# Kernel optimization log

Measured on AMD Instinct MI355X. Metric: run time of the kernel, lower is better.

The kernel has to match this reference:

```python
import jax, jax.numpy as jnp
import numpy as np


def setup_inputs() -> dict:
    key = jax.random.key(0)
    k1, k2 = jax.random.split(key)
    B, C, H, W = 8, 19, 512, 1024
    inputs = jax.random.normal(k1, (B, C, H, W), dtype=jnp.float32)
    targets = jax.random.randint(k2, (B, H, W), 0, C, dtype=jnp.int32)
    return {"inputs": inputs, "targets": targets}


def reference(inputs, targets):
    # inputs: [B, C, H, W] logits; targets: [B, H, W] int class ids
    C = inputs.shape[1]
    logp = jax.nn.log_softmax(inputs, axis=1)            # [B, C, H, W]
    t = targets.reshape(-1)                              # [N]
    # per-class inverse-frequency weights via single-pass histogram
    counts = jnp.zeros((C,), dtype=jnp.float32).at[t].add(1.0)
    inv_freq = jnp.where(counts > 0, 1.0 / jnp.maximum(counts, 1.0), 1.0)  # [C]
    weight = inv_freq[t]                                 # [N]
    # gather log-prob of the target class per pixel
    logp_flat = jnp.transpose(logp, (0, 2, 3, 1)).reshape(-1, C)  # [N, C]
    nll = -jnp.take_along_axis(logp_flat, t[:, None], axis=1)[:, 0]  # [N]
    return jnp.sum(weight * nll) / jnp.sum(weight)
```

## Files before the change

kernel.cpp:

```cpp
#include <hip/hip_runtime.h>

#define NUM_C 19
#define HW_SHIFT 19
#define HW (1 << HW_SHIFT)
#define NPIX (8 * HW)
#define NGROUPS (NPIX / 4)

__global__ __launch_bounds__(256) void ifl_main(const float* __restrict__ x,
                                                const int* __restrict__ tgt,
                                                float* __restrict__ ws) {
    __shared__ float red[2 * NUM_C];
    if (threadIdx.x < 2 * NUM_C) red[threadIdx.x] = 0.0f;
    __syncthreads();

    float acc[NUM_C];
    float cnt[NUM_C];
#pragma unroll
    for (int c = 0; c < NUM_C; ++c) { acc[c] = 0.0f; cnt[c] = 0.0f; }

    const int tid = blockIdx.x * blockDim.x + threadIdx.x;
    const int nthreads = gridDim.x * blockDim.x;

    union F4 { float4 q; float f[4]; };
    union I4 { int4 q; int i[4]; };

    for (int g = tid; g < NGROUPS; g += nthreads) {
        const int p = g << 2;
        const int b = p >> HW_SHIFT;
        const int r = p & (HW - 1);
        const float4* base4 =
            reinterpret_cast<const float4*>(x + ((size_t)(b * NUM_C) << HW_SHIFT) + r);

        F4 v[NUM_C];
#pragma unroll
        for (int c = 0; c < NUM_C; ++c) v[c].q = base4[(size_t)c << (HW_SHIFT - 2)];

        I4 tt;
        tt.q = *reinterpret_cast<const int4*>(tgt + p);

#pragma unroll
        for (int k = 0; k < 4; ++k) {
            const int tg = tt.i[k];
            float m = v[0].f[k];
#pragma unroll
            for (int c = 1; c < NUM_C; ++c) m = fmaxf(m, v[c].f[k]);
            float s = 0.0f;
#pragma unroll
            for (int c = 0; c < NUM_C; ++c) s += __expf(v[c].f[k] - m);
            float xt = v[0].f[k];
#pragma unroll
            for (int c = 1; c < NUM_C; ++c) xt = (tg == c) ? v[c].f[k] : xt;
            const float nll = m + __logf(s) - xt;
#pragma unroll
            for (int c = 0; c < NUM_C; ++c) {
                const bool h = (tg == c);
                acc[c] += h ? nll : 0.0f;
                cnt[c] += h ? 1.0f : 0.0f;
            }
        }
    }

#pragma unroll
    for (int c = 0; c < NUM_C; ++c) {
        float a = acc[c];
        float n = cnt[c];
#pragma unroll
        for (int off = 32; off > 0; off >>= 1) {
            a += __shfl_down(a, off, 64);
            n += __shfl_down(n, off, 64);
        }
        if ((threadIdx.x & 63) == 0) {
            atomicAdd(&red[c], a);
            atomicAdd(&red[NUM_C + c], n);
        }
    }
    __syncthreads();

    if (threadIdx.x < 2 * NUM_C) atomicAdd(&ws[threadIdx.x], red[threadIdx.x]);
}

__global__ void ifl_final(const float* __restrict__ ws, float* __restrict__ out) {
    if (threadIdx.x == 0) {
        float num = 0.0f, den = 0.0f;
#pragma unroll
        for (int c = 0; c < NUM_C; ++c) {
            const float cn = ws[NUM_C + c];
            const float inv = (cn > 0.0f) ? (1.0f / fmaxf(cn, 1.0f)) : 1.0f;
            num += inv * ws[c];
            den += inv * cn;
        }
        out[0] = num / den;
    }
}

extern "C" void kernel_launch(void* const* d_in, const int* in_sizes, int n_in,
                              void* d_out, int out_size, void* d_ws, size_t ws_size,
                              hipStream_t stream) {
    const float* x = (const float*)d_in[0];
    const int* tgt = (const int*)d_in[1];
    float* ws = (float*)d_ws;
    float* out = (float*)d_out;

    hipMemsetAsync(ws, 0, 2 * NUM_C * sizeof(float), stream);

    ifl_main<<<2048, 256, 0, stream>>>(x, tgt, ws);
    ifl_final<<<1, 64, 0, stream>>>(ws, out);
}
```

Measured before the change: 440.3 us.

## Drop max-subtraction in log-softmax and give each thread 8 pixels in a flat grid

```diff
diff --git a/kernel.cpp b/kernel.cpp
--- a/kernel.cpp
+++ b/kernel.cpp
@@ -5,58 +5,56 @@
 #define HW (1 << HW_SHIFT)
 #define NPIX (8 * HW)
 #define NGROUPS (NPIX / 4)
+#define BLOCK 256
+#define GPT 2
+#define NBLOCKS (NGROUPS / (BLOCK * GPT))
 
-__global__ __launch_bounds__(256) void ifl_main(const float* __restrict__ x,
-                                                const int* __restrict__ tgt,
-                                                float* __restrict__ ws) {
+
+__global__ __launch_bounds__(BLOCK, 4) void ifl_main(const float* __restrict__ x,
+                                                     const int* __restrict__ tgt,
+                                                     float* __restrict__ ws) {
     __shared__ float red[2 * NUM_C];
     if (threadIdx.x < 2 * NUM_C) red[threadIdx.x] = 0.0f;
     __syncthreads();
 
-    float acc[NUM_C];
-    float cnt[NUM_C];
+    const int tid = blockIdx.x * BLOCK + threadIdx.x;
+    const int p   = (tid * GPT) << 2;
+    const int b   = p >> HW_SHIFT;
+    const int r   = p & (HW - 1);
+    const float* base = x + (((size_t)b * NUM_C) << HW_SHIFT) + r;
+
+    const int4 t0 = *reinterpret_cast<const int4*>(tgt + p);
+    const int4 t1 = *reinterpret_cast<const int4*>(tgt + p + 4);
+    const int tg[8] = {t0.x, t0.y, t0.z, t0.w, t1.x, t1.y, t1.z, t1.w};
+
+    float s[8], xt[8];
+#pragma unroll
+    for (int k = 0; k < 8; ++k) { s[k] = 0.0f; xt[k] = 0.0f; }
+
+#pragma unroll
+    for (int c = 0; c < NUM_C; ++c) {
+        const float4 va = *reinterpret_cast<const float4*>(base + ((size_t)c << HW_SHIFT));
+        const float4 vb = *reinterpret_cast<const float4*>(base + ((size_t)c << HW_SHIFT) + 4);
+        const float v[8] = {va.x, va.y, va.z, va.w, vb.x, vb.y, vb.z, vb.w};
+#pragma unroll
+        for (int k = 0; k < 8; ++k) {
+            s[k] += __expf(v[k]);
+            xt[k] = (tg[k] == c) ? v[k] : xt[k];
+        }
+    }
+
+    float acc[NUM_C], cnt[NUM_C];
 #pragma unroll
     for (int c = 0; c < NUM_C; ++c) { acc[c] = 0.0f; cnt[c] = 0.0f; }
 
-    const int tid = blockIdx.x * blockDim.x + threadIdx.x;
-    const int nthreads = gridDim.x * blockDim.x;
-
-    union F4 { float4 q; float f[4]; };
-    union I4 { int4 q; int i[4]; };
-
-    for (int g = tid; g < NGROUPS; g += nthreads) {
-        const int p = g << 2;
-        const int b = p >> HW_SHIFT;
-        const int r = p & (HW - 1);
-        const float4* base4 =
-            reinterpret_cast<const float4*>(x + ((size_t)(b * NUM_C) << HW_SHIFT) + r);
-
-        F4 v[NUM_C];
 #pragma unroll
-        for (int c = 0; c < NUM_C; ++c) v[c].q = base4[(size_t)c << (HW_SHIFT - 2)];
-
-        I4 tt;
-        tt.q = *reinterpret_cast<const int4*>(tgt + p);
-
+    for (int k = 0; k < 8; ++k) {
+        const float nll = __logf(s[k]) - xt[k];
 #pragma unroll
-        for (int k = 0; k < 4; ++k) {
-            const int tg = tt.i[k];
-            float m = v[0].f[k];
-#pragma unroll
-            for (int c = 1; c < NUM_C; ++c) m = fmaxf(m, v[c].f[k]);
-            float s = 0.0f;
-#pragma unroll
-            for (int c = 0; c < NUM_C; ++c) s += __expf(v[c].f[k] - m);
-            float xt = v[0].f[k];
-#pragma unroll
-            for (int c = 1; c < NUM_C; ++c) xt = (tg == c) ? v[c].f[k] : xt;
-            const float nll = m + __logf(s) - xt;
-#pragma unroll
-            for (int c = 0; c < NUM_C; ++c) {
-                const bool h = (tg == c);
-                acc[c] += h ? nll : 0.0f;
-                cnt[c] += h ? 1.0f : 0.0f;
-            }
+        for (int c = 0; c < NUM_C; ++c) {
+            const bool h = (tg[k] == c);
+            acc[c] += h ? nll : 0.0f;
+            cnt[c] += h ? 1.0f : 0.0f;
         }
     }
 
@@ -103,6 +101,6 @@
 
     hipMemsetAsync(ws, 0, 2 * NUM_C * sizeof(float), stream);
 
-    ifl_main<<<2048, 256, 0, stream>>>(x, tgt, ws);
+    ifl_main<<<NBLOCKS, BLOCK, 0, stream>>>(x, tgt, ws);
     ifl_final<<<1, 64, 0, stream>>>(ws, out);
 }
```

Result: slower. 453.5 us (+3.0%).
